# Performance work log

Hardware: AMD Instinct MI355X
Metric: run time of the kernel (lower is better)

## Reference

```python
import jax, jax.numpy as jnp
import numpy as np

B, Q, K, H, D = 4, 256, 256, 768, 768
NUM_LEN = 100  # length_embedding rows


def setup_inputs() -> dict:
    key = jax.random.key(0)
    ks = jax.random.split(key, 9)
    q = jax.random.normal(ks[0], (B, Q, H), jnp.float32)
    k = jax.random.normal(ks[1], (B, K, H), jnp.float32)
    m = jax.random.normal(ks[2], (B, K, D), jnp.float32)
    length_mask = jax.random.randint(ks[3], (B, Q, K), 0, NUM_LEN)
    attention_mask = jax.random.uniform(ks[4], (B, Q, K), jnp.float32)
    emb = jax.random.normal(ks[5], (NUM_LEN, H), jnp.float32) * 0.02
    # xavier-uniform-ish init for the two small Linears
    W1 = jax.random.normal(ks[6], (1, H), jnp.float32) * (1.0 / np.sqrt(H))
    b1 = jnp.zeros((1,), jnp.float32)
    W2 = jax.random.normal(ks[7], (5, H), jnp.float32) * (1.0 / np.sqrt(H))
    b2 = jnp.zeros((5,), jnp.float32)
    return {"q": q, "k": k, "m": m, "attention_mask": attention_mask,
            "emb": emb, "W1": W1, "b1": b1, "W2": W2, "b2": b2,
            "length_mask": length_mask}


def reference(q, k, m, attention_mask, emb, W1, b1, W2, b2, length_mask):
    # broadcast-add: q[B,Q,1,H] + k[B,1,K,H] + length_embedding[length_mask] -> [B,Q,K,H]
    s = q[:, :, None, :] + k[:, None, :, :] + emb[length_mask]
    # att_liner: H -> 1, squeezed -> [B,Q,K]
    attention_scores = jnp.einsum('bqkh,h->bqk', s, W1[0]) + b1[0]
    # att2_liner: H -> 5, softmax over the 5 classes -> [B,Q,K,5]
    scores = jax.nn.softmax(jnp.einsum('bqkh,ch->bqkc', s, W2) + b2, axis=-1)
    # multiplicative mask, then softmax over K
    attention_scores = attention_scores * attention_mask
    attention_probs = jax.nn.softmax(attention_scores, axis=-1)
    # dropout(p=0.2) is identity in eval mode
    attention_content = jnp.einsum('bqk,bkd->bqd', attention_probs, m)
    return attention_content, scores
```

## Files before the change

### kernel.cpp

```cpp
#include <hip/hip_runtime.h>

#define Hn 768
#define Bn 4
#define Qn 256
#define Kn 256
#define Dn 768
#define WS_KP 8192
#define WS_EP 16384

typedef float f32x2 __attribute__((ext_vector_type(2)));

__device__ __forceinline__ void pkfma_lo(f32x2& acc, f32x2 p, f32x2 mm) {
    asm("v_pk_fma_f32 %0, %1, %2, %0 op_sel:[0,0,0] op_sel_hi:[0,1,1]"
        : "+v"(acc) : "v"(p), "v"(mm));
}
__device__ __forceinline__ void pkfma_hi(f32x2& acc, f32x2 p, f32x2 mm) {
    asm("v_pk_fma_f32 %0, %1, %2, %0 op_sel:[1,0,0] op_sel_hi:[1,1,1]"
        : "+v"(acc) : "v"(p), "v"(mm));
}

__global__ __launch_bounds__(256) void proj_kernel(
    const float* __restrict__ q, const float* __restrict__ k,
    const float* __restrict__ emb, const float* __restrict__ W1,
    const float* __restrict__ W2, float* __restrict__ ws)
{
    int wid  = blockIdx.x * 4 + (threadIdx.x >> 6);
    int lane = threadIdx.x & 63;
    const float* src;
    float* dst;
    if (wid < 1024)      { src = q + wid * Hn;            dst = ws + wid * 8; }
    else if (wid < 2048) { src = k + (wid - 1024) * Hn;   dst = ws + WS_KP + (wid - 1024) * 8; }
    else {
        int r = wid - 2048;
        if (r >= 100) return;
        src = emb + r * Hn; dst = ws + WS_EP + r * 8;
    }
    float acc[6] = {0.f, 0.f, 0.f, 0.f, 0.f, 0.f};
    #pragma unroll
    for (int i = 0; i < 3; ++i) {
        int h = i * 256 + lane * 4;
        float4 x  = *(const float4*)&src[h];
        float4 w1 = *(const float4*)&W1[h];
        acc[0] += x.x * w1.x + x.y * w1.y + x.z * w1.z + x.w * w1.w;
        #pragma unroll
        for (int c = 0; c < 5; ++c) {
            float4 w2 = *(const float4*)&W2[c * Hn + h];
            acc[1 + c] += x.x * w2.x + x.y * w2.y + x.z * w2.z + x.w * w2.w;
        }
    }
    #pragma unroll
    for (int j = 0; j < 6; ++j) {
        float v = acc[j];
        #pragma unroll
        for (int off = 32; off > 0; off >>= 1)
            v += __shfl_xor(v, off, 64);
        if (lane == 0) dst[j] = v;
    }
}

__global__ __launch_bounds__(256, 4) void fused_kernel(
    const float* __restrict__ ws_proj, const float* __restrict__ m,
    const float* __restrict__ am, const int* __restrict__ lm,
    const float* __restrict__ b1, const float* __restrict__ b2,
    float* __restrict__ scores_out, float* __restrict__ content_out)
{
    __shared__ float p[8][Kn];
    __shared__ float4 parts[8][8][32];

    int bid = blockIdx.x;
    int dt = bid % 6;
    int qt = (bid / 6) & 31;
    int b  = bid / 192;
    int q0 = qt * 8;
    int t = threadIdx.x;
    int wave = t >> 6, lane = t & 63;

    const float* qP = ws_proj;
    const float* kP = ws_proj + WS_KP;
    const float* eP = ws_proj + WS_EP;

    int kh = t >> 5;
    int c4 = t & 31;
    const float* mb0 = m + (size_t)(b * Kn + (kh << 5)) * Dn + dt * 128 + (c4 << 2);
    float4 pm0 = *(const float4*)(mb0);
    float4 pm1 = *(const float4*)(mb0 + Dn);
    float4 pm2 = *(const float4*)(mb0 + 2 * Dn);
    float4 pm3 = *(const float4*)(mb0 + 3 * Dn);
    float4 pm4 = *(const float4*)(mb0 + 4 * Dn);
    float4 pm5 = *(const float4*)(mb0 + 5 * Dn);
    float4 pm6 = *(const float4*)(mb0 + 6 * Dn);
    float4 pm7 = *(const float4*)(mb0 + 7 * Dn);

    float b1v = b1[0];
    float b2v[5] = {b2[0], b2[1], b2[2], b2[3], b2[4]};

    int slo = dt * 43;
    int shi = (dt == 5) ? 256 : slo + 43;

    float kp[4][6];
    #pragma unroll
    for (int j = 0; j < 4; ++j) {
        const float* kr = &kP[(b * Kn + j * 64 + lane) * 8];
        float4 a  = *(const float4*)kr;
        float4 bb = *(const float4*)(kr + 4);
        kp[j][0] = a.x; kp[j][1] = a.y; kp[j][2] = a.z;
        kp[j][3] = a.w; kp[j][4] = bb.x; kp[j][5] = bb.y;
    }

    #pragma unroll
    for (int rr = 0; rr < 2; ++rr) {
        int qi = wave + rr * 4;
        int bq = b * Qn + q0 + qi;
        float qp[6];
        #pragma unroll
        for (int j2 = 0; j2 < 6; ++j2) qp[j2] = qP[bq * 8 + j2];

        int   l[4];
        float as[4];
        #pragma unroll
        for (int j = 0; j < 4; ++j) {
            int kk = j * 64 + lane;
            l[j] = lm[(size_t)bq * Kn + kk];
            float e0  = eP[l[j] * 8];
            float amv = am[(size_t)bq * Kn + kk];
            as[j] = (qp[0] + kp[j][0] + e0 + b1v) * amv;
        }
        float mx = fmaxf(fmaxf(as[0], as[1]), fmaxf(as[2], as[3]));
        #pragma unroll
        for (int off = 32; off > 0; off >>= 1)
            mx = fmaxf(mx, __shfl_xor(mx, off, 64));
        float e[4], sum = 0.f;
        #pragma unroll
        for (int j = 0; j < 4; ++j) { e[j] = __expf(as[j] - mx); sum += e[j]; }
        #pragma unroll
        for (int off = 32; off > 0; off >>= 1)
            sum += __shfl_xor(sum, off, 64);
        float inv = 1.f / sum;
        #pragma unroll
        for (int j = 0; j < 4; ++j) p[qi][j * 64 + lane] = e[j] * inv;

        #pragma unroll
        for (int j = 0; j < 4; ++j) {
            int kk = j * 64 + lane;
            if (kk >= slo && kk < shi) {
                const float* er = &eP[l[j] * 8];
                float4 ea = *(const float4*)er;
                float4 eb = *(const float4*)(er + 4);
                float epc[5] = {ea.y, ea.z, ea.w, eb.x, eb.y};
                float lg[5];
                float mx5 = -1e30f;
                #pragma unroll
                for (int c = 0; c < 5; ++c) {
                    lg[c] = qp[c + 1] + kp[j][c + 1] + epc[c] + b2v[c];
                    mx5 = fmaxf(mx5, lg[c]);
                }
                float s5 = 0.f;
                #pragma unroll
                for (int c = 0; c < 5; ++c) { lg[c] = __expf(lg[c] - mx5); s5 += lg[c]; }
                float inv5 = 1.f / s5;
                float* so = scores_out + ((size_t)bq * Kn + kk) * 5;
                #pragma unroll
                for (int c = 0; c < 5; ++c) so[c] = lg[c] * inv5;
            }
        }
    }
    __syncthreads();

    f32x2 accA[8], accB[8];
    #pragma unroll
    for (int qi = 0; qi < 8; ++qi) {
        accA[qi] = (f32x2){0.f, 0.f};
        accB[qi] = (f32x2){0.f, 0.f};
    }

    #pragma unroll
    for (int g = 0; g < 8; ++g) {
        int k0 = (kh << 5) + (g << 2);
        float4 m0, m1, m2, m3;
        if (g == 0)      { m0 = pm0; m1 = pm1; m2 = pm2; m3 = pm3; }
        else if (g == 1) { m0 = pm4; m1 = pm5; m2 = pm6; m3 = pm7; }
        else {
            const float* mb = m + (size_t)(b * Kn + k0) * Dn + dt * 128 + (c4 << 2);
            m0 = *(const float4*)(mb);
            m1 = *(const float4*)(mb + Dn);
            m2 = *(const float4*)(mb + 2 * Dn);
            m3 = *(const float4*)(mb + 3 * Dn);
        }
        f32x2 m0A = {m0.x, m0.y}, m0B = {m0.z, m0.w};
        f32x2 m1A = {m1.x, m1.y}, m1B = {m1.z, m1.w};
        f32x2 m2A = {m2.x, m2.y}, m2B = {m2.z, m2.w};
        f32x2 m3A = {m3.x, m3.y}, m3B = {m3.z, m3.w};
        #pragma unroll
        for (int qi = 0; qi < 8; ++qi) {
            float4 pv = *(const float4*)&p[qi][k0];
            f32x2 p01 = {pv.x, pv.y};
            f32x2 p23 = {pv.z, pv.w};
            pkfma_lo(accA[qi], p01, m0A); pkfma_lo(accB[qi], p01, m0B);
            pkfma_hi(accA[qi], p01, m1A); pkfma_hi(accB[qi], p01, m1B);
            pkfma_lo(accA[qi], p23, m2A); pkfma_lo(accB[qi], p23, m2B);
            pkfma_hi(accA[qi], p23, m3A); pkfma_hi(accB[qi], p23, m3B);
        }
    }
    #pragma unroll
    for (int qi = 0; qi < 8; ++qi) {
        float4 v;
        v.x = accA[qi][0]; v.y = accA[qi][1];
        v.z = accB[qi][0]; v.w = accB[qi][1];
        parts[kh][qi][c4] = v;
    }
    __syncthreads();

    int qi2 = t >> 5, c42 = t & 31;
    float4 s = parts[0][qi2][c42];
    #pragma unroll
    for (int kk = 1; kk < 8; ++kk) {
        float4 v = parts[kk][qi2][c42];
        s.x += v.x; s.y += v.y; s.z += v.z; s.w += v.w;
    }
    *(float4*)(content_out + (size_t)(b * Qn + q0 + qi2) * Dn + dt * 128 + (c42 << 2)) = s;
}

extern "C" void kernel_launch(void* const* d_in, const int* in_sizes, int n_in,
                              void* d_out, int out_size, void* d_ws, size_t ws_size,
                              hipStream_t stream) {
    const float* q   = (const float*)d_in[0];
    const float* k   = (const float*)d_in[1];
    const float* m   = (const float*)d_in[2];
    const float* am  = (const float*)d_in[3];
    const float* emb = (const float*)d_in[4];
    const float* W1  = (const float*)d_in[5];
    const float* b1  = (const float*)d_in[6];
    const float* W2  = (const float*)d_in[7];
    const float* b2  = (const float*)d_in[8];
    const int*   lm  = (const int*)d_in[9];

    float* out         = (float*)d_out;
    float* out_content = out;
    float* out_scores  = out + Bn * Qn * Dn;

    float* ws = (float*)d_ws;

    proj_kernel<<<537, 256, 0, stream>>>(q, k, emb, W1, W2, ws);
    fused_kernel<<<Bn * (Qn / 8) * 6, 256, 0, stream>>>(
        ws, m, am, lm, b1, b2, out_scores, out_content);
}
```

Baseline: 22.77 us.

## Double fused block to 512 threads and drop softmax max subtraction

The fused kernel now runs 512 threads per block. Each of the 8 waves computes one query row's softmax, and the probability-times-m product is split across 16 k-groups of 16 keys. Partial sums from paired half-waves are combined with a cross-lane shuffle before the shared-memory reduction. Both softmaxes also skip the max-subtraction pass to shorten the dependency chain, which can overflow for large logits. The launch bound of (512,4) tightens the register budget, which may cause spills.

```diff
diff --git a/kernel.cpp b/kernel.cpp
--- a/kernel.cpp
+++ b/kernel.cpp
@@ -58,7 +58,7 @@
     }
 }
 
-__global__ __launch_bounds__(256, 4) void fused_kernel(
+__global__ __launch_bounds__(512, 4) void fused_kernel(
     const float* __restrict__ ws_proj, const float* __restrict__ m,
     const float* __restrict__ am, const int* __restrict__ lm,
     const float* __restrict__ b1, const float* __restrict__ b2,
@@ -81,15 +81,11 @@
 
     int kh = t >> 5;
     int c4 = t & 31;
-    const float* mb0 = m + (size_t)(b * Kn + (kh << 5)) * Dn + dt * 128 + (c4 << 2);
+    const float* mb0 = m + (size_t)(b * Kn + kh * 16) * Dn + dt * 128 + (c4 << 2);
     float4 pm0 = *(const float4*)(mb0);
     float4 pm1 = *(const float4*)(mb0 + Dn);
     float4 pm2 = *(const float4*)(mb0 + 2 * Dn);
     float4 pm3 = *(const float4*)(mb0 + 3 * Dn);
-    float4 pm4 = *(const float4*)(mb0 + 4 * Dn);
-    float4 pm5 = *(const float4*)(mb0 + 5 * Dn);
-    float4 pm6 = *(const float4*)(mb0 + 6 * Dn);
-    float4 pm7 = *(const float4*)(mb0 + 7 * Dn);
 
     float b1v = b1[0];
     float b2v[5] = {b2[0], b2[1], b2[2], b2[3], b2[4]};
@@ -107,31 +103,26 @@
         kp[j][3] = a.w; kp[j][4] = bb.x; kp[j][5] = bb.y;
     }
 
-    #pragma unroll
-    for (int rr = 0; rr < 2; ++rr) {
-        int qi = wave + rr * 4;
+    {
+        int qi = wave;
         int bq = b * Qn + q0 + qi;
         float qp[6];
         #pragma unroll
         for (int j2 = 0; j2 < 6; ++j2) qp[j2] = qP[bq * 8 + j2];
 
         int   l[4];
-        float as[4];
+        float e[4];
+        float sum = 0.f;
         #pragma unroll
         for (int j = 0; j < 4; ++j) {
             int kk = j * 64 + lane;
             l[j] = lm[(size_t)bq * Kn + kk];
             float e0  = eP[l[j] * 8];
             float amv = am[(size_t)bq * Kn + kk];
-            as[j] = (qp[0] + kp[j][0] + e0 + b1v) * amv;
-        }
-        float mx = fmaxf(fmaxf(as[0], as[1]), fmaxf(as[2], as[3]));
-        #pragma unroll
-        for (int off = 32; off > 0; off >>= 1)
-            mx = fmaxf(mx, __shfl_xor(mx, off, 64));
-        float e[4], sum = 0.f;
-        #pragma unroll
-        for (int j = 0; j < 4; ++j) { e[j] = __expf(as[j] - mx); sum += e[j]; }
+            float as  = (qp[0] + kp[j][0] + e0 + b1v) * amv;
+            e[j] = __expf(as);
+            sum += e[j];
+        }
         #pragma unroll
         for (int off = 32; off > 0; off >>= 1)
             sum += __shfl_xor(sum, off, 64);
@@ -148,15 +139,12 @@
                 float4 eb = *(const float4*)(er + 4);
                 float epc[5] = {ea.y, ea.z, ea.w, eb.x, eb.y};
                 float lg[5];
-                float mx5 = -1e30f;
+                float s5 = 0.f;
                 #pragma unroll
                 for (int c = 0; c < 5; ++c) {
-                    lg[c] = qp[c + 1] + kp[j][c + 1] + epc[c] + b2v[c];
-                    mx5 = fmaxf(mx5, lg[c]);
+                    lg[c] = __expf(qp[c + 1] + kp[j][c + 1] + epc[c] + b2v[c]);
+                    s5 += lg[c];
                 }
-                float s5 = 0.f;
-                #pragma unroll
-                for (int c = 0; c < 5; ++c) { lg[c] = __expf(lg[c] - mx5); s5 += lg[c]; }
                 float inv5 = 1.f / s5;
                 float* so = scores_out + ((size_t)bq * Kn + kk) * 5;
                 #pragma unroll
@@ -174,11 +162,10 @@
     }
 
     #pragma unroll
-    for (int g = 0; g < 8; ++g) {
-        int k0 = (kh << 5) + (g << 2);
+    for (int g = 0; g < 4; ++g) {
+        int k0 = kh * 16 + (g << 2);
         float4 m0, m1, m2, m3;
-        if (g == 0)      { m0 = pm0; m1 = pm1; m2 = pm2; m3 = pm3; }
-        else if (g == 1) { m0 = pm4; m1 = pm5; m2 = pm6; m3 = pm7; }
+        if (g == 0) { m0 = pm0; m1 = pm1; m2 = pm2; m3 = pm3; }
         else {
             const float* mb = m + (size_t)(b * Kn + k0) * Dn + dt * 128 + (c4 << 2);
             m0 = *(const float4*)(mb);
@@ -201,23 +188,35 @@
             pkfma_hi(accA[qi], p23, m3A); pkfma_hi(accB[qi], p23, m3B);
         }
     }
+
     #pragma unroll
     for (int qi = 0; qi < 8; ++qi) {
-        float4 v;
-        v.x = accA[qi][0]; v.y = accA[qi][1];
-        v.z = accB[qi][0]; v.w = accB[qi][1];
-        parts[kh][qi][c4] = v;
+        accA[qi][0] += __shfl_xor(accA[qi][0], 32, 64);
+        accA[qi][1] += __shfl_xor(accA[qi][1], 32, 64);
+        accB[qi][0] += __shfl_xor(accB[qi][0], 32, 64);
+        accB[qi][1] += __shfl_xor(accB[qi][1], 32, 64);
+    }
+    if (lane < 32) {
+        #pragma unroll
+        for (int qi = 0; qi < 8; ++qi) {
+            float4 v;
+            v.x = accA[qi][0]; v.y = accA[qi][1];
+            v.z = accB[qi][0]; v.w = accB[qi][1];
+            parts[wave][qi][c4] = v;
+        }
     }
     __syncthreads();
 
-    int qi2 = t >> 5, c42 = t & 31;
-    float4 s = parts[0][qi2][c42];
-    #pragma unroll
-    for (int kk = 1; kk < 8; ++kk) {
-        float4 v = parts[kk][qi2][c42];
-        s.x += v.x; s.y += v.y; s.z += v.z; s.w += v.w;
-    }
-    *(float4*)(content_out + (size_t)(b * Qn + q0 + qi2) * Dn + dt * 128 + (c42 << 2)) = s;
+    if (t < 256) {
+        int qi2 = t >> 5, c42 = t & 31;
+        float4 s = parts[0][qi2][c42];
+        #pragma unroll
+        for (int kk = 1; kk < 8; ++kk) {
+            float4 v = parts[kk][qi2][c42];
+            s.x += v.x; s.y += v.y; s.z += v.z; s.w += v.w;
+        }
+        *(float4*)(content_out + (size_t)(b * Qn + q0 + qi2) * Dn + dt * 128 + (c42 << 2)) = s;
+    }
 }
 
 extern "C" void kernel_launch(void* const* d_in, const int* in_sizes, int n_in,
@@ -241,6 +240,6 @@
     float* ws = (float*)d_ws;
 
     proj_kernel<<<537, 256, 0, stream>>>(q, k, emb, W1, W2, ws);
-    fused_kernel<<<Bn * (Qn / 8) * 6, 256, 0, stream>>>(
+    fused_kernel<<<Bn * (Qn / 8) * 6, 512, 0, stream>>>(
         ws, m, am, lm, b1, b2, out_scores, out_content);
 }
```

New measurement: 25.12 us. 10.3% more time.
